# Kernel optimization log

Measured on AMD Instinct MI355X. Metric: run time of the kernel, lower is better.

Reference implementation:

```python
import jax, jax.numpy as jnp
import numpy as np

B, T, N = 8, 1024, 1024
R, NR = 8, 128          # regions, neurons per region (N = R*NR)
D = 512                 # d_model


def setup_inputs() -> dict:
    key = jax.random.key(0)
    ks = jax.random.split(key, 6)
    spikes = jax.random.normal(ks[0], (B, T, N), dtype=jnp.float32)
    # region assignment: random permutation of neuron ids split into R groups
    perm = jax.random.permutation(ks[1], N)
    region_indices = perm.reshape(R, NR).astype(jnp.int32)
    # per-region Linear(NR -> D) stored already transposed for gathered layout
    W_enc = jax.random.normal(ks[2], (R, NR, D), dtype=jnp.float32) / np.sqrt(NR)
    b_enc = jax.random.normal(ks[3], (R, D), dtype=jnp.float32) * 0.02
    # per-region Linear(D -> NR)
    W_dec = jax.random.normal(ks[4], (R, D, NR), dtype=jnp.float32) / np.sqrt(D)
    b_dec = jax.random.normal(ks[5], (R, NR), dtype=jnp.float32) * 0.02
    return {"spikes": spikes, "W_enc": W_enc, "b_enc": b_enc,
            "W_dec": W_dec, "b_dec": b_dec, "region_indices": region_indices}


def reference(spikes, W_enc, b_enc, W_dec, b_dec, region_indices):
    # gather: per-region channel subsets  [B,T,R,NR]
    x_r = spikes[:, :, region_indices]
    # RegionEncoder: Linear(NR -> D) per region  [B,T,R,D]
    tokens = jnp.einsum('btrn,rnd->btrd', x_r, W_enc) + b_enc
    # RegionDecoder: Linear(D -> NR) per region  [B,T,R,NR]
    y = jnp.einsum('btrd,rdn->btrn', tokens, W_dec) + b_dec
    # scatter back into full neuron axis (index_copy_ on dim 2)
    flat_idx = region_indices.reshape(-1)          # [N], a permutation
    out = jnp.zeros_like(spikes).at[:, :, flat_idx].set(y.reshape(spikes.shape[0], spikes.shape[1], -1))
    return out
```

## Files before the change

### kernel.cpp

```cpp
#include <hip/hip_runtime.h>
#include <hip/hip_bf16.h>


typedef __attribute__((ext_vector_type(8))) short bf16x8;
typedef __attribute__((ext_vector_type(4))) float f32x4;
typedef __attribute__((ext_vector_type(4))) short s16x4;

#define NREG 8
#define NRD  128
#define DD   512
#define NN   1024
#define ROWS 16

static __device__ __forceinline__ unsigned short f2bf(float x) {
  union { float f; unsigned u; } v; v.f = x;
  unsigned r = v.u + 0x7fffu + ((v.u >> 16) & 1u);
  return (unsigned short)(r >> 16);
}
static __device__ __forceinline__ unsigned short f2bf_hw(float x) {
  union { __hip_bfloat16 h; unsigned short u; } c;
  c.h = __float2bfloat16(x);
  return c.u;
}
static __device__ __forceinline__ float bf2f(unsigned short b) {
  union { unsigned u; float f; } v; v.u = ((unsigned)b) << 16;
  return v.f;
}

__global__ __launch_bounds__(256) void prep1_kernel(
    const float* __restrict__ W_enc, const float* __restrict__ b_enc,
    const float* __restrict__ W_dec, const int* __restrict__ idx,
    int* __restrict__ pos_ws, float* __restrict__ part,
    float* __restrict__ part_c)
{
  __shared__ unsigned short As[128 * 128];
  __shared__ unsigned short Bs[128 * 128];
  int blk = blockIdx.x, t = threadIdx.x;

  if (blk < 32) {
    int r = blk >> 2, dc = blk & 3, d0 = dc * 128;
    const float* We = W_enc + (size_t)r * NRD * DD;
    const float* Wd = W_dec + (size_t)r * DD * NRD;
    const float* be = b_enc + (size_t)r * DD;

    int n4 = (t & 31) * 4, dlb = t >> 5;
    float c0 = 0.f, c1 = 0.f, c2 = 0.f, c3 = 0.f;
    #pragma unroll
    for (int p = 0; p < 16; ++p) {
      int dl = dlb + p * 8;
      float4 v = *(const float4*)&Wd[(size_t)(d0 + dl) * NRD + n4];
      float bev = be[d0 + dl];
      As[(n4 + 0) * 128 + (dl ^ (((n4 + 0) & 7) << 3))] = f2bf(v.x);
      As[(n4 + 1) * 128 + (dl ^ (((n4 + 1) & 7) << 3))] = f2bf(v.y);
      As[(n4 + 2) * 128 + (dl ^ (((n4 + 2) & 7) << 3))] = f2bf(v.z);
      As[(n4 + 3) * 128 + (dl ^ (((n4 + 3) & 7) << 3))] = f2bf(v.w);
      c0 += v.x * bev; c1 += v.y * bev; c2 += v.z * bev; c3 += v.w * bev;
    }
    {
      float4 cv; cv.x = c0; cv.y = c1; cv.z = c2; cv.w = c3;
      *(float4*)&part_c[((size_t)(r * 4 + dc) * 8 + dlb) * 128 + n4] = cv;
    }
    #pragma unroll
    for (int i = 0; i < 8; ++i) {
      int cid = t + i * 256;
      int k = cid >> 4, dq = (cid & 15) * 8;
      const float* src = &We[(size_t)k * DD + d0 + dq];
      float4 u = *(const float4*)src;
      float4 u2 = *(const float4*)(src + 4);
      bf16x8 pk;
      pk[0] = (short)f2bf(u.x);  pk[1] = (short)f2bf(u.y);
      pk[2] = (short)f2bf(u.z);  pk[3] = (short)f2bf(u.w);
      pk[4] = (short)f2bf(u2.x); pk[5] = (short)f2bf(u2.y);
      pk[6] = (short)f2bf(u2.z); pk[7] = (short)f2bf(u2.w);
      *(bf16x8*)&Bs[k * 128 + (dq ^ ((k & 7) << 3))] = pk;
    }
    __syncthreads();

    int lane = t & 63, w = t >> 6;
    int arow = lane & 15, ag = lane >> 4;
    f32x4 acc[8][2];
    #pragma unroll
    for (int i = 0; i < 8; ++i) {
      acc[i][0] = (f32x4){0.f, 0.f, 0.f, 0.f};
      acc[i][1] = (f32x4){0.f, 0.f, 0.f, 0.f};
    }
    #pragma unroll
    for (int nt = 0; nt < 8; ++nt) {
      int nl = nt * 16 + arow, asw = (nl & 7) << 3;
      bf16x8 a[4];
      #pragma unroll
      for (int ks = 0; ks < 4; ++ks)
        a[ks] = *(const bf16x8*)&As[nl * 128 + ((ks * 32 + ag * 8) ^ asw)];
      #pragma unroll
      for (int kt = 0; kt < 2; ++kt) {
        int kk = w * 32 + kt * 16 + arow, bsw = (kk & 7) << 3;
        #pragma unroll
        for (int ks = 0; ks < 4; ++ks) {
          bf16x8 b = *(const bf16x8*)&Bs[kk * 128 + ((ks * 32 + ag * 8) ^ bsw)];
          acc[nt][kt] = __builtin_amdgcn_mfma_f32_16x16x32_bf16(a[ks], b, acc[nt][kt], 0, 0, 0);
        }
      }
    }
    float* dst = part + (size_t)(r * 4 + dc) * 16384;
    #pragma unroll
    for (int nt = 0; nt < 8; ++nt)
      #pragma unroll
      for (int kt = 0; kt < 2; ++kt)
        #pragma unroll
        for (int v = 0; v < 4; ++v)
          dst[(nt * 16 + ag * 4 + v) * 128 + (w * 32 + kt * 16 + arow)] = acc[nt][kt][v];
  } else {
    #pragma unroll
    for (int i = 0; i < 4; ++i) {
      int q = t * 4 + i;
      pos_ws[idx[q]] = q;
    }
  }
}

__global__ __launch_bounds__(256) void prep2_kernel(
    const float* __restrict__ part, const float* __restrict__ part_c,
    const float* __restrict__ b_dec, unsigned short* __restrict__ MTp,
    float* __restrict__ c_ws)
{
  int blk = blockIdx.x, t = threadIdx.x;
  if (blk < 128) {
    int e0 = (blk * 256 + t) * 4;
    int r = e0 >> 14, off = e0 & 16383;
    int n = off >> 7, k0 = off & 127;
    const float* p = part + (size_t)r * 4 * 16384 + off;
    float4 s0 = *(const float4*)&p[0];
    float4 s1 = *(const float4*)&p[16384];
    float4 s2 = *(const float4*)&p[32768];
    float4 s3 = *(const float4*)&p[49152];
    s16x4 o;
    o.x = (short)f2bf(s0.x + s1.x + s2.x + s3.x);
    o.y = (short)f2bf(s0.y + s1.y + s2.y + s3.y);
    o.z = (short)f2bf(s0.z + s1.z + s2.z + s3.z);
    o.w = (short)f2bf(s0.w + s1.w + s2.w + s3.w);
    int w = n >> 4, arow = n & 15, kt = k0 >> 5, ag = (k0 >> 3) & 3, sub = k0 & 7;
    int chunk = (r * 32 + w * 4 + kt) * 64 + (arow * 4 + ag);
    *(s16x4*)&MTp[chunk * 8 + sub] = o;
  } else if (blk < 132) {
    int e = (blk - 128) * 256 + t;
    int n = e & 127;
    int r = e >> 7;
    float s = b_dec[e];
    #pragma unroll
    for (int dc = 0; dc < 4; ++dc)
      #pragma unroll
      for (int g = 0; g < 8; ++g)
        s += part_c[((size_t)(r * 4 + dc) * 8 + g) * 128 + n];
    c_ws[e] = s;
  }
}

__global__ __launch_bounds__(512) void codec_kernel(
    const float* __restrict__ spikes, const int* __restrict__ pos_ws,
    const float* __restrict__ c_ws, const unsigned short* __restrict__ MTp,
    const int* __restrict__ idx, float* __restrict__ out)
{
  __shared__ unsigned short Xs[ROWS * NN];
  __shared__ unsigned short Ys[ROWS * NN];
  int t = threadIdx.x;
  int w = t >> 6, lane = t & 63;
  int arow = lane & 15, ag = lane >> 4;
  int n0 = w * 16 + arow;
  int lanechunk = arow * 4 + ag;
  size_t row0 = (size_t)blockIdx.x * ROWS;

  int4 p4c[4];
  #pragma unroll
  for (int ch = 0; ch < 4; ++ch)
    p4c[ch] = *(const int4*)&pos_ws[ch * 256 + lane * 4];
  float cv[NREG];
  int col[NREG];
  #pragma unroll
  for (int r = 0; r < NREG; ++r) {
    cv[r]  = c_ws[r * 128 + n0];
    col[r] = idx[r * 128 + n0];
  }

  #pragma unroll
  for (int ch = 0; ch < 4; ++ch) {
    int j = ch * 256 + lane * 4;
    int4 p4 = p4c[ch];
    #pragma unroll
    for (int rl = 0; rl < 2; ++rl) {
      int row = w * 2 + rl;
      float4 v = *(const float4*)&spikes[(row0 + row) * NN + j];
      int base = row * NN, sw = (row & 7) << 3;
      Xs[base + (p4.x ^ sw)] = f2bf_hw(v.x);
      Xs[base + (p4.y ^ sw)] = f2bf_hw(v.y);
      Xs[base + (p4.z ^ sw)] = f2bf_hw(v.z);
      Xs[base + (p4.w ^ sw)] = f2bf_hw(v.w);
    }
  }
  __syncthreads();

  const bf16x8* Bb = (const bf16x8*)MTp;
  int asw = (arow & 7) << 3;
  bf16x8 bb[2][4];
  #pragma unroll
  for (int kt = 0; kt < 4; ++kt)
    bb[0][kt] = Bb[(w * 4 + kt) * 64 + lanechunk];
  #pragma unroll
  for (int r = 0; r < NREG; ++r) {
    if (r < NREG - 1) {
      #pragma unroll
      for (int kt = 0; kt < 4; ++kt)
        bb[(r + 1) & 1][kt] = Bb[((r + 1) * 32 + w * 4 + kt) * 64 + lanechunk];
    }
    bf16x8 a[4];
    #pragma unroll
    for (int kt = 0; kt < 4; ++kt)
      a[kt] = *(const bf16x8*)&Xs[arow * NN + ((r * 128 + kt * 32 + ag * 8) ^ asw)];
    f32x4 acc = {0.f, 0.f, 0.f, 0.f};
    #pragma unroll
    for (int kt = 0; kt < 4; ++kt)
      acc = __builtin_amdgcn_mfma_f32_16x16x32_bf16(a[kt], bb[r & 1][kt], acc, 0, 0, 0);
    #pragma unroll
    for (int v = 0; v < 4; ++v) {
      int i = ag * 4 + v, isw = (i & 7) << 3;
      Ys[i * NN + (col[r] ^ isw)] = f2bf_hw(acc[v] + cv[r]);
    }
  }
  __syncthreads();

  #pragma unroll
  for (int ch = 0; ch < 4; ++ch) {
    int j = ch * 256 + lane * 4;
    #pragma unroll
    for (int rl = 0; rl < 2; ++rl) {
      int row = w * 2 + rl;
      int sw = (row & 7) << 3;
      s16x4 y = *(const s16x4*)&Ys[row * NN + (j ^ sw)];
      float4 v;
      v.x = bf2f((unsigned short)y.x);
      v.y = bf2f((unsigned short)y.y);
      v.z = bf2f((unsigned short)y.z);
      v.w = bf2f((unsigned short)y.w);
      *(float4*)&out[(row0 + row) * NN + j] = v;
    }
  }
}

extern "C" void kernel_launch(void* const* d_in, const int* in_sizes, int n_in,
                              void* d_out, int out_size, void* d_ws, size_t ws_size,
                              hipStream_t stream) {
  const float* spikes = (const float*)d_in[0];
  const float* W_enc  = (const float*)d_in[1];
  const float* b_enc  = (const float*)d_in[2];
  const float* W_dec  = (const float*)d_in[3];
  const float* b_dec  = (const float*)d_in[4];
  const int*   idx    = (const int*)d_in[5];
  float* out = (float*)d_out;

  char* ws = (char*)d_ws;
  int*            pos_ws  = (int*)ws;
  float*          c_ws    = (float*)(ws + 4096);
  unsigned short* MTp_ws  = (unsigned short*)(ws + 8192);
  float*          part    = (float*)(ws + 270336);
  float*          part_c  = (float*)(ws + 2367488);

  prep1_kernel<<<33, 256, 0, stream>>>(W_enc, b_enc, W_dec, idx,
                                       pos_ws, part, part_c);
  prep2_kernel<<<132, 256, 0, stream>>>(part, part_c, b_dec, MTp_ws, c_ws);
  codec_kernel<<<8192 / ROWS, 512, 0, stream>>>(spikes, pos_ws, c_ws, MTp_ws, idx, out);
}
```

Before: 32.65 us.

## Double codec block to 1024 threads, splitting regions across two wave groups

```diff
diff --git a/kernel.cpp b/kernel.cpp
--- a/kernel.cpp
+++ b/kernel.cpp
@@ -155,7 +155,7 @@
   }
 }
 
-__global__ __launch_bounds__(512) void codec_kernel(
+__global__ __launch_bounds__(1024) void codec_kernel(
     const float* __restrict__ spikes, const int* __restrict__ pos_ws,
     const float* __restrict__ c_ws, const unsigned short* __restrict__ MTp,
     const int* __restrict__ idx, float* __restrict__ out)
@@ -164,8 +164,9 @@
   __shared__ unsigned short Ys[ROWS * NN];
   int t = threadIdx.x;
   int w = t >> 6, lane = t & 63;
+  int wg = w >> 3, wcol = w & 7;
   int arow = lane & 15, ag = lane >> 4;
-  int n0 = w * 16 + arow;
+  int n0 = wcol * 16 + arow;
   int lanechunk = arow * 4 + ag;
   size_t row0 = (size_t)blockIdx.x * ROWS;
 
@@ -173,23 +174,22 @@
   #pragma unroll
   for (int ch = 0; ch < 4; ++ch)
     p4c[ch] = *(const int4*)&pos_ws[ch * 256 + lane * 4];
-  float cv[NREG];
-  int col[NREG];
+  float cv[4];
+  int col[4];
   #pragma unroll
-  for (int r = 0; r < NREG; ++r) {
-    cv[r]  = c_ws[r * 128 + n0];
-    col[r] = idx[r * 128 + n0];
-  }
-
-  #pragma unroll
-  for (int ch = 0; ch < 4; ++ch) {
-    int j = ch * 256 + lane * 4;
-    int4 p4 = p4c[ch];
-    #pragma unroll
-    for (int rl = 0; rl < 2; ++rl) {
-      int row = w * 2 + rl;
-      float4 v = *(const float4*)&spikes[(row0 + row) * NN + j];
-      int base = row * NN, sw = (row & 7) << 3;
+  for (int q = 0; q < 4; ++q) {
+    int r = wg * 4 + q;
+    cv[q]  = c_ws[r * 128 + n0];
+    col[q] = idx[r * 128 + n0];
+  }
+
+  {
+    int base = w * NN, sw = (w & 7) << 3;
+    #pragma unroll
+    for (int ch = 0; ch < 4; ++ch) {
+      int j = ch * 256 + lane * 4;
+      float4 v = *(const float4*)&spikes[(row0 + w) * NN + j];
+      int4 p4 = p4c[ch];
       Xs[base + (p4.x ^ sw)] = f2bf_hw(v.x);
       Xs[base + (p4.y ^ sw)] = f2bf_hw(v.y);
       Xs[base + (p4.z ^ sw)] = f2bf_hw(v.z);
@@ -200,47 +200,40 @@
 
   const bf16x8* Bb = (const bf16x8*)MTp;
   int asw = (arow & 7) << 3;
-  bf16x8 bb[2][4];
   #pragma unroll
-  for (int kt = 0; kt < 4; ++kt)
-    bb[0][kt] = Bb[(w * 4 + kt) * 64 + lanechunk];
-  #pragma unroll
-  for (int r = 0; r < NREG; ++r) {
-    if (r < NREG - 1) {
-      #pragma unroll
-      for (int kt = 0; kt < 4; ++kt)
-        bb[(r + 1) & 1][kt] = Bb[((r + 1) * 32 + w * 4 + kt) * 64 + lanechunk];
-    }
-    bf16x8 a[4];
+  for (int q = 0; q < 4; ++q) {
+    int r = wg * 4 + q;
+    bf16x8 b[4], a[4];
+    #pragma unroll
+    for (int kt = 0; kt < 4; ++kt)
+      b[kt] = Bb[(r * 32 + wcol * 4 + kt) * 64 + lanechunk];
     #pragma unroll
     for (int kt = 0; kt < 4; ++kt)
       a[kt] = *(const bf16x8*)&Xs[arow * NN + ((r * 128 + kt * 32 + ag * 8) ^ asw)];
     f32x4 acc = {0.f, 0.f, 0.f, 0.f};
     #pragma unroll
     for (int kt = 0; kt < 4; ++kt)
-      acc = __builtin_amdgcn_mfma_f32_16x16x32_bf16(a[kt], bb[r & 1][kt], acc, 0, 0, 0);
+      acc = __builtin_amdgcn_mfma_f32_16x16x32_bf16(a[kt], b[kt], acc, 0, 0, 0);
     #pragma unroll
     for (int v = 0; v < 4; ++v) {
       int i = ag * 4 + v, isw = (i & 7) << 3;
-      Ys[i * NN + (col[r] ^ isw)] = f2bf_hw(acc[v] + cv[r]);
+      Ys[i * NN + (col[q] ^ isw)] = f2bf_hw(acc[v] + cv[q]);
     }
   }
   __syncthreads();
 
-  #pragma unroll
-  for (int ch = 0; ch < 4; ++ch) {
-    int j = ch * 256 + lane * 4;
-    #pragma unroll
-    for (int rl = 0; rl < 2; ++rl) {
-      int row = w * 2 + rl;
-      int sw = (row & 7) << 3;
-      s16x4 y = *(const s16x4*)&Ys[row * NN + (j ^ sw)];
+  {
+    int sw = (w & 7) << 3;
+    #pragma unroll
+    for (int ch = 0; ch < 4; ++ch) {
+      int j = ch * 256 + lane * 4;
+      s16x4 y = *(const s16x4*)&Ys[w * NN + (j ^ sw)];
       float4 v;
       v.x = bf2f((unsigned short)y.x);
       v.y = bf2f((unsigned short)y.y);
       v.z = bf2f((unsigned short)y.z);
       v.w = bf2f((unsigned short)y.w);
-      *(float4*)&out[(row0 + row) * NN + j] = v;
+      *(float4*)&out[(row0 + w) * NN + j] = v;
     }
   }
 }
@@ -266,5 +259,5 @@
   prep1_kernel<<<33, 256, 0, stream>>>(W_enc, b_enc, W_dec, idx,
                                        pos_ws, part, part_c);
   prep2_kernel<<<132, 256, 0, stream>>>(part, part_c, b_dec, MTp_ws, c_ws);
-  codec_kernel<<<8192 / ROWS, 512, 0, stream>>>(spikes, pos_ws, c_ws, MTp_ws, idx, out);
-}
+  codec_kernel<<<8192 / ROWS, 1024, 0, stream>>>(spikes, pos_ws, c_ws, MTp_ws, idx, out);
+}
```

New measurement: 32.56 us. Within noise of the previous version (-0.3%).

## Reuse Xs for outputs, halve block size, two MFMA tiles per wave

Applied to the files above, without the earlier changes.

```diff
diff --git a/kernel.cpp b/kernel.cpp
--- a/kernel.cpp
+++ b/kernel.cpp
@@ -155,17 +155,16 @@
   }
 }
 
-__global__ __launch_bounds__(512) void codec_kernel(
+__global__ __launch_bounds__(256) void codec_kernel(
     const float* __restrict__ spikes, const int* __restrict__ pos_ws,
     const float* __restrict__ c_ws, const unsigned short* __restrict__ MTp,
-    const int* __restrict__ idx, float* __restrict__ out)
+    float* __restrict__ out)
 {
   __shared__ unsigned short Xs[ROWS * NN];
-  __shared__ unsigned short Ys[ROWS * NN];
   int t = threadIdx.x;
   int w = t >> 6, lane = t & 63;
   int arow = lane & 15, ag = lane >> 4;
-  int n0 = w * 16 + arow;
+  int n0 = w * 32 + arow;
   int lanechunk = arow * 4 + ag;
   size_t row0 = (size_t)blockIdx.x * ROWS;
 
@@ -173,21 +172,14 @@
   #pragma unroll
   for (int ch = 0; ch < 4; ++ch)
     p4c[ch] = *(const int4*)&pos_ws[ch * 256 + lane * 4];
-  float cv[NREG];
-  int col[NREG];
-  #pragma unroll
-  for (int r = 0; r < NREG; ++r) {
-    cv[r]  = c_ws[r * 128 + n0];
-    col[r] = idx[r * 128 + n0];
-  }
 
   #pragma unroll
   for (int ch = 0; ch < 4; ++ch) {
     int j = ch * 256 + lane * 4;
     int4 p4 = p4c[ch];
     #pragma unroll
-    for (int rl = 0; rl < 2; ++rl) {
-      int row = w * 2 + rl;
+    for (int rl = 0; rl < 4; ++rl) {
+      int row = w * 4 + rl;
       float4 v = *(const float4*)&spikes[(row0 + row) * NN + j];
       int base = row * NN, sw = (row & 7) << 3;
       Xs[base + (p4.x ^ sw)] = f2bf_hw(v.x);
@@ -200,29 +192,30 @@
 
   const bf16x8* Bb = (const bf16x8*)MTp;
   int asw = (arow & 7) << 3;
-  bf16x8 bb[2][4];
-  #pragma unroll
-  for (int kt = 0; kt < 4; ++kt)
-    bb[0][kt] = Bb[(w * 4 + kt) * 64 + lanechunk];
-  #pragma unroll
   for (int r = 0; r < NREG; ++r) {
-    if (r < NREG - 1) {
-      #pragma unroll
-      for (int kt = 0; kt < 4; ++kt)
-        bb[(r + 1) & 1][kt] = Bb[((r + 1) * 32 + w * 4 + kt) * 64 + lanechunk];
-    }
-    bf16x8 a[4];
+    float cvA = c_ws[r * 128 + n0];
+    float cvB = c_ws[r * 128 + n0 + 16];
+    bf16x8 b0[4], b1[4], a[4];
+    #pragma unroll
+    for (int kt = 0; kt < 4; ++kt) {
+      b0[kt] = Bb[(r * 32 + (2 * w) * 4 + kt) * 64 + lanechunk];
+      b1[kt] = Bb[(r * 32 + (2 * w + 1) * 4 + kt) * 64 + lanechunk];
+    }
     #pragma unroll
     for (int kt = 0; kt < 4; ++kt)
       a[kt] = *(const bf16x8*)&Xs[arow * NN + ((r * 128 + kt * 32 + ag * 8) ^ asw)];
-    f32x4 acc = {0.f, 0.f, 0.f, 0.f};
-    #pragma unroll
-    for (int kt = 0; kt < 4; ++kt)
-      acc = __builtin_amdgcn_mfma_f32_16x16x32_bf16(a[kt], bb[r & 1][kt], acc, 0, 0, 0);
+    f32x4 acc0 = {0.f, 0.f, 0.f, 0.f}, acc1 = {0.f, 0.f, 0.f, 0.f};
+    #pragma unroll
+    for (int kt = 0; kt < 4; ++kt) {
+      acc0 = __builtin_amdgcn_mfma_f32_16x16x32_bf16(a[kt], b0[kt], acc0, 0, 0, 0);
+      acc1 = __builtin_amdgcn_mfma_f32_16x16x32_bf16(a[kt], b1[kt], acc1, 0, 0, 0);
+    }
+    __syncthreads();
     #pragma unroll
     for (int v = 0; v < 4; ++v) {
-      int i = ag * 4 + v, isw = (i & 7) << 3;
-      Ys[i * NN + (col[r] ^ isw)] = f2bf_hw(acc[v] + cv[r]);
+      int i = ag * 4 + v, isw = (i & 7) << 3, ib = i * NN;
+      Xs[ib + ((r * 128 + n0) ^ isw)]      = f2bf_hw(acc0[v] + cvA);
+      Xs[ib + ((r * 128 + n0 + 16) ^ isw)] = f2bf_hw(acc1[v] + cvB);
     }
   }
   __syncthreads();
@@ -230,16 +223,16 @@
   #pragma unroll
   for (int ch = 0; ch < 4; ++ch) {
     int j = ch * 256 + lane * 4;
-    #pragma unroll
-    for (int rl = 0; rl < 2; ++rl) {
-      int row = w * 2 + rl;
-      int sw = (row & 7) << 3;
-      s16x4 y = *(const s16x4*)&Ys[row * NN + (j ^ sw)];
+    int4 p4 = p4c[ch];
+    #pragma unroll
+    for (int rl = 0; rl < 4; ++rl) {
+      int row = w * 4 + rl;
+      int base = row * NN, sw = (row & 7) << 3;
       float4 v;
-      v.x = bf2f((unsigned short)y.x);
-      v.y = bf2f((unsigned short)y.y);
-      v.z = bf2f((unsigned short)y.z);
-      v.w = bf2f((unsigned short)y.w);
+      v.x = bf2f(Xs[base + (p4.x ^ sw)]);
+      v.y = bf2f(Xs[base + (p4.y ^ sw)]);
+      v.z = bf2f(Xs[base + (p4.z ^ sw)]);
+      v.w = bf2f(Xs[base + (p4.w ^ sw)]);
       *(float4*)&out[(row0 + row) * NN + j] = v;
     }
   }
@@ -266,5 +259,5 @@
   prep1_kernel<<<33, 256, 0, stream>>>(W_enc, b_enc, W_dec, idx,
                                        pos_ws, part, part_c);
   prep2_kernel<<<132, 256, 0, stream>>>(part, part_c, b_dec, MTp_ws, c_ws);
-  codec_kernel<<<8192 / ROWS, 512, 0, stream>>>(spikes, pos_ws, c_ws, MTp_ws, idx, out);
-}
+  codec_kernel<<<8192 / ROWS, 256, 0, stream>>>(spikes, pos_ws, c_ws, MTp_ws, out);
+}
```

Result: slower. 34.63 us (+6.1%).

## Assign regions to waves and reuse Xs for outputs, dropping Ys buffer

Applied to the files above, without the earlier changes.

```diff
diff --git a/kernel.cpp b/kernel.cpp
--- a/kernel.cpp
+++ b/kernel.cpp
@@ -158,14 +158,13 @@
 __global__ __launch_bounds__(512) void codec_kernel(
     const float* __restrict__ spikes, const int* __restrict__ pos_ws,
     const float* __restrict__ c_ws, const unsigned short* __restrict__ MTp,
-    const int* __restrict__ idx, float* __restrict__ out)
+    float* __restrict__ out)
 {
   __shared__ unsigned short Xs[ROWS * NN];
-  __shared__ unsigned short Ys[ROWS * NN];
   int t = threadIdx.x;
   int w = t >> 6, lane = t & 63;
   int arow = lane & 15, ag = lane >> 4;
-  int n0 = w * 16 + arow;
+  int asw = (arow & 7) << 3;
   int lanechunk = arow * 4 + ag;
   size_t row0 = (size_t)blockIdx.x * ROWS;
 
@@ -173,13 +172,10 @@
   #pragma unroll
   for (int ch = 0; ch < 4; ++ch)
     p4c[ch] = *(const int4*)&pos_ws[ch * 256 + lane * 4];
-  float cv[NREG];
-  int col[NREG];
-  #pragma unroll
-  for (int r = 0; r < NREG; ++r) {
-    cv[r]  = c_ws[r * 128 + n0];
-    col[r] = idx[r * 128 + n0];
-  }
+  float cvr[8];
+  #pragma unroll
+  for (int j = 0; j < 8; ++j)
+    cvr[j] = c_ws[w * 128 + j * 16 + arow];
 
   #pragma unroll
   for (int ch = 0; ch < 4; ++ch) {
@@ -198,31 +194,26 @@
   }
   __syncthreads();
 
+  bf16x8 a[4];
+  #pragma unroll
+  for (int kt = 0; kt < 4; ++kt)
+    a[kt] = *(const bf16x8*)&Xs[arow * NN + ((w * 128 + kt * 32 + ag * 8) ^ asw)];
   const bf16x8* Bb = (const bf16x8*)MTp;
-  int asw = (arow & 7) << 3;
-  bf16x8 bb[2][4];
-  #pragma unroll
-  for (int kt = 0; kt < 4; ++kt)
-    bb[0][kt] = Bb[(w * 4 + kt) * 64 + lanechunk];
-  #pragma unroll
-  for (int r = 0; r < NREG; ++r) {
-    if (r < NREG - 1) {
-      #pragma unroll
-      for (int kt = 0; kt < 4; ++kt)
-        bb[(r + 1) & 1][kt] = Bb[((r + 1) * 32 + w * 4 + kt) * 64 + lanechunk];
-    }
-    bf16x8 a[4];
+  #pragma unroll
+  for (int j = 0; j < 8; ++j) {
+    bf16x8 b[4];
     #pragma unroll
     for (int kt = 0; kt < 4; ++kt)
-      a[kt] = *(const bf16x8*)&Xs[arow * NN + ((r * 128 + kt * 32 + ag * 8) ^ asw)];
+      b[kt] = Bb[(w * 32 + j * 4 + kt) * 64 + lanechunk];
     f32x4 acc = {0.f, 0.f, 0.f, 0.f};
     #pragma unroll
     for (int kt = 0; kt < 4; ++kt)
-      acc = __builtin_amdgcn_mfma_f32_16x16x32_bf16(a[kt], bb[r & 1][kt], acc, 0, 0, 0);
+      acc = __builtin_amdgcn_mfma_f32_16x16x32_bf16(a[kt], b[kt], acc, 0, 0, 0);
+    int coln = w * 128 + j * 16 + arow;
     #pragma unroll
     for (int v = 0; v < 4; ++v) {
       int i = ag * 4 + v, isw = (i & 7) << 3;
-      Ys[i * NN + (col[r] ^ isw)] = f2bf_hw(acc[v] + cv[r]);
+      Xs[i * NN + (coln ^ isw)] = f2bf_hw(acc[v] + cvr[j]);
     }
   }
   __syncthreads();
@@ -230,16 +221,16 @@
   #pragma unroll
   for (int ch = 0; ch < 4; ++ch) {
     int j = ch * 256 + lane * 4;
+    int4 p4 = p4c[ch];
     #pragma unroll
     for (int rl = 0; rl < 2; ++rl) {
       int row = w * 2 + rl;
-      int sw = (row & 7) << 3;
-      s16x4 y = *(const s16x4*)&Ys[row * NN + (j ^ sw)];
+      int base = row * NN, sw = (row & 7) << 3;
       float4 v;
-      v.x = bf2f((unsigned short)y.x);
-      v.y = bf2f((unsigned short)y.y);
-      v.z = bf2f((unsigned short)y.z);
-      v.w = bf2f((unsigned short)y.w);
+      v.x = bf2f(Xs[base + (p4.x ^ sw)]);
+      v.y = bf2f(Xs[base + (p4.y ^ sw)]);
+      v.z = bf2f(Xs[base + (p4.z ^ sw)]);
+      v.w = bf2f(Xs[base + (p4.w ^ sw)]);
       *(float4*)&out[(row0 + row) * NN + j] = v;
     }
   }
@@ -266,5 +257,5 @@
   prep1_kernel<<<33, 256, 0, stream>>>(W_enc, b_enc, W_dec, idx,
                                        pos_ws, part, part_c);
   prep2_kernel<<<132, 256, 0, stream>>>(part, part_c, b_dec, MTp_ws, c_ws);
-  codec_kernel<<<8192 / ROWS, 512, 0, stream>>>(spikes, pos_ws, c_ws, MTp_ws, idx, out);
-}
+  codec_kernel<<<8192 / ROWS, 512, 0, stream>>>(spikes, pos_ws, c_ws, MTp_ws, out);
+}
```

Result: slower. 33.56 us (+2.8%).
